# Optimization experiments

Measured on AMD Instinct MI355X. Metric: run time of the kernel, lower is better.

The kernel has to match this reference:

```python
import jax, jax.numpy as jnp
import numpy as np

B, S, D, H = 4, 2048, 1024, 16
HD = D // H  # head_size = 64


def setup_inputs() -> dict:
    key = jax.random.key(0)
    ks = jax.random.split(key, 9)
    sc = 0.02
    x = jax.random.normal(ks[0], (B, S, D), dtype=jnp.float32)
    Wq = jax.random.normal(ks[1], (H, D, HD), dtype=jnp.float32) * sc
    Wk = jax.random.normal(ks[2], (H, D, HD), dtype=jnp.float32) * sc
    Wv = jax.random.normal(ks[3], (H, D, HD), dtype=jnp.float32) * sc
    bq = jax.random.normal(ks[4], (H, HD), dtype=jnp.float32) * sc
    bk = jax.random.normal(ks[5], (H, HD), dtype=jnp.float32) * sc
    bv = jax.random.normal(ks[6], (H, HD), dtype=jnp.float32) * sc
    Wp = jax.random.normal(ks[7], (D, D), dtype=jnp.float32) * sc
    bp = jax.random.normal(ks[8], (D,), dtype=jnp.float32) * sc
    return {"x": x, "Wq": Wq, "bq": bq, "Wk": Wk, "bk": bk,
            "Wv": Wv, "bv": bv, "Wp": Wp, "bp": bp}


def reference(x, Wq, bq, Wk, bk, Wv, bv, Wp, bp):
    # Per-head Linear q/k/v, batched over heads with einsum (equivalent math
    # to the original Python loop over SingleHeadAttention modules).
    q = jnp.einsum('bsd,hde->bhse', x, Wq) + bq[None, :, None, :]
    k = jnp.einsum('bsd,hde->bhse', x, Wk) + bk[None, :, None, :]
    v = jnp.einsum('bsd,hde->bhse', x, Wv) + bv[None, :, None, :]
    att = jnp.einsum('bhqe,bhke->bhqk', q, k) / jnp.sqrt(jnp.asarray(HD, q.dtype))
    causal = jnp.tril(jnp.ones((S, S), dtype=bool))  # [S,S]
    att = jnp.where(causal[None, None], att, jnp.finfo(att.dtype).min)
    w = jax.nn.softmax(att, axis=-1)
    o = jnp.einsum('bhqk,bhke->bhqe', w, v)           # [B,H,S,HD]
    o = o.transpose(0, 2, 1, 3).reshape(B, S, D)      # concat heads on last dim
    # output projection; dropout is identity in eval (p=0.0)
    return jnp.einsum('bsd,de->bse', o, Wp) + bp
```

## Files before the change

### kernel.cpp

```cpp
#include <hip/hip_runtime.h>
#include <hip/hip_bf16.h>

typedef __attribute__((ext_vector_type(8)))  short bf16x8;
typedef __attribute__((ext_vector_type(4)))  float f32x4;
typedef __attribute__((ext_vector_type(16))) float f32x16;
typedef __attribute__((ext_vector_type(2)))  int   i32x2;

#define NH  16
#define HD  64
#define SEQ 2048
#define DM  1024
#define NB  4

#define QSCALE 0.18033688011112042f

#define MFMA(a,b,c)   __builtin_amdgcn_mfma_f32_16x16x32_bf16((a),(b),(c),0,0,0)
#define MFMA32(a,b,c) __builtin_amdgcn_mfma_f32_32x32x16_bf16((a),(b),(c),0,0,0)

static __device__ __forceinline__ void gload_lds16(const void* g, void* l) {
    __builtin_amdgcn_global_load_lds(
        (const __attribute__((address_space(1))) void*)g,
        (__attribute__((address_space(3))) void*)l, 16, 0, 0);
}

__global__ __launch_bounds__(256)
void prep(const float* __restrict__ x,  const float* __restrict__ Wq,
          const float* __restrict__ Wk, const float* __restrict__ Wv,
          const float* __restrict__ Wp,
          __hip_bfloat16* __restrict__ xb,  __hip_bfloat16* __restrict__ wqt,
          __hip_bfloat16* __restrict__ wkt, __hip_bfloat16* __restrict__ wvt,
          __hip_bfloat16* __restrict__ wpt) {
    const long XE = (long)NB * SEQ * DM;
    const long CAST_T = XE / 8;
    long gid = (long)blockIdx.x * 256 + threadIdx.x;
    if (gid < CAST_T) {
        long i = gid * 8;
        float4 a = *reinterpret_cast<const float4*>(x + i);
        float4 b = *reinterpret_cast<const float4*>(x + i + 4);
        ushort4 o1, o2;
        o1.x = __bfloat16_as_ushort(__float2bfloat16(a.x));
        o1.y = __bfloat16_as_ushort(__float2bfloat16(a.y));
        o1.z = __bfloat16_as_ushort(__float2bfloat16(a.z));
        o1.w = __bfloat16_as_ushort(__float2bfloat16(a.w));
        o2.x = __bfloat16_as_ushort(__float2bfloat16(b.x));
        o2.y = __bfloat16_as_ushort(__float2bfloat16(b.y));
        o2.z = __bfloat16_as_ushort(__float2bfloat16(b.z));
        o2.w = __bfloat16_as_ushort(__float2bfloat16(b.w));
        *reinterpret_cast<ushort4*>(xb + i)     = o1;
        *reinterpret_cast<ushort4*>(xb + i + 4) = o2;
        return;
    }
    long r = gid - CAST_T;
    const long WQK = 1 << 20;
    if (r < 3 * WQK) {
        int z = (int)(r >> 20);
        long idx = r & (WQK - 1);
        const float* src = (z == 0) ? Wq : (z == 1) ? Wk : Wv;
        __hip_bfloat16* dst = (z == 0) ? wqt : (z == 1) ? wkt : wvt;
        int c  = (int)(idx & 63);
        long t2 = idx >> 6;
        int rr = (int)(t2 & 1023);
        int mm = (int)(t2 >> 10);
        dst[((long)mm * HD + c) * DM + rr] = __float2bfloat16(src[idx]);
    } else {
        long idx = r - 3 * WQK;
        int c  = (int)(idx & 1023);
        int rr = (int)(idx >> 10);
        wpt[(long)c * DM + rr] = __float2bfloat16(Wp[idx]);
    }
}

__global__ __launch_bounds__(256)
void qkv_gemm(const __hip_bfloat16* __restrict__ A,
              const __hip_bfloat16* __restrict__ BT,
              const float* __restrict__ b0,
              const float* __restrict__ b1,
              const float* __restrict__ b2,
              __hip_bfloat16* __restrict__ Qo,
              __hip_bfloat16* __restrict__ Ko,
              __hip_bfloat16* __restrict__ Vto) {
    __shared__ __align__(16) char lds[2][32768];
    int tid = threadIdx.x;
    int w = tid >> 6, l = tid & 63;
    int lr = l & 15, lg = l >> 4;
    int wr = w >> 1, wc = w & 1;
    int mtile = blockIdx.x, ntile = blockIdx.y;
    const int AR0 = mtile * 128, BR0 = ntile * 128;

    const int rsub = w * 8 + (l >> 3);
    const int sg0 = l & 7;
    auto stage = [&](const __hip_bfloat16* g, int grow0, int kc, char* lbase) {
#pragma unroll
        for (int i = 0; i < 4; ++i) {
            int row = i * 32 + rsub;
            gload_lds16(g + (long)(grow0 + row) * DM + kc + ((sg0 ^ (row & 7)) << 3),
                        lbase + i * 4096 + w * 1024);
        }
    };

    int aoff[4][2], boff[4][2];
#pragma unroll
    for (int m = 0; m < 4; ++m) {
        int ra = wr * 64 + m * 16 + lr;
        int rb = wc * 64 + m * 16 + lr;
#pragma unroll
        for (int kh = 0; kh < 2; ++kh) {
            aoff[m][kh] = ra * 128 + (((kh * 4 + lg) ^ (ra & 7)) << 4);
            boff[m][kh] = 16384 + rb * 128 + (((kh * 4 + lg) ^ (rb & 7)) << 4);
        }
    }

    f32x4 acc[4][4] = {};

    stage(A,  AR0, 0, lds[0]);
    stage(BT, BR0, 0, lds[0] + 16384);
    __syncthreads();

    int cur = 0;
    for (int kt = 0; kt < 16; ++kt) {
        if (kt < 15) {
            int kc = (kt + 1) * 64;
            stage(A,  AR0, kc, lds[cur ^ 1]);
            stage(BT, BR0, kc, lds[cur ^ 1] + 16384);
        }
        bf16x8 bf[4][2];
#pragma unroll
        for (int n = 0; n < 4; ++n) {
            bf[n][0] = *(const bf16x8*)(lds[cur] + boff[n][0]);
            bf[n][1] = *(const bf16x8*)(lds[cur] + boff[n][1]);
        }
#pragma unroll
        for (int m = 0; m < 4; ++m) {
            bf16x8 a0 = *(const bf16x8*)(lds[cur] + aoff[m][0]);
            bf16x8 a1 = *(const bf16x8*)(lds[cur] + aoff[m][1]);
#pragma unroll
            for (int n = 0; n < 4; ++n) {
                acc[m][n] = MFMA(a0, bf[n][0], acc[m][n]);
                acc[m][n] = MFMA(a1, bf[n][1], acc[m][n]);
            }
        }
        __syncthreads();
        cur ^= 1;
    }

    int z = ntile >> 3;
    const float* bias = (z == 0) ? b0 : (z == 1) ? b1 : b2;
    int colbase = (ntile & 7) * 128 + wc * 64;
#pragma unroll
    for (int n = 0; n < 4; ++n) {
        int hc = colbase + n * 16 + lr;
        int h = hc >> 6, e = hc & 63;
        float bb = bias[hc];
#pragma unroll
        for (int m = 0; m < 4; ++m) {
            int row0 = mtile * 128 + wr * 64 + m * 16 + lg * 4;
            int b = row0 >> 11, s0 = row0 & 2047;
            if (z == 0) {
#pragma unroll
                for (int r = 0; r < 4; ++r)
                    Qo[(((long)b * NH + h) * SEQ + s0 + r) * HD + e] =
                        __float2bfloat16((acc[m][n][r] + bb) * QSCALE);
            } else if (z == 1) {
#pragma unroll
                for (int r = 0; r < 4; ++r)
                    Ko[(((long)b * NH + h) * SEQ + s0 + r) * HD + e] =
                        __float2bfloat16(acc[m][n][r] + bb);
            } else {
                ushort4 s4;
                s4.x = __bfloat16_as_ushort(__float2bfloat16(acc[m][n][0] + bb));
                s4.y = __bfloat16_as_ushort(__float2bfloat16(acc[m][n][1] + bb));
                s4.z = __bfloat16_as_ushort(__float2bfloat16(acc[m][n][2] + bb));
                s4.w = __bfloat16_as_ushort(__float2bfloat16(acc[m][n][3] + bb));
                *reinterpret_cast<ushort4*>(
                    Vto + ((long)(b * NH + h) * HD + e) * SEQ + s0) = s4;
            }
        }
    }
}

__global__ __launch_bounds__(256)
void out_gemm(const __hip_bfloat16* __restrict__ A,
              const __hip_bfloat16* __restrict__ BT,
              const float* __restrict__ b0,
              float* __restrict__ Fo) {
    __shared__ __align__(16) char smem[2][16384];
    int tid = threadIdx.x;
    int w = tid >> 6, l = tid & 63;
    int wr = w >> 1, wc = w & 1;
    int lr = l & 15, lg = l >> 4;
    int mtile = blockIdx.x, ntile = blockIdx.y;

    const __hip_bfloat16* Ab = A  + (long)mtile * 128 * DM;
    const __hip_bfloat16* Bb = BT + (long)ntile * 128 * DM;

    const int srow0 = tid >> 2;
    const int srow1 = 64 + srow0;
    const int g0 = (tid & 3) ^ ((srow0 >> 1) & 3);

    int aoff[4], boff[4];
#pragma unroll
    for (int m = 0; m < 4; ++m) {
        int ra = wr * 64 + m * 16 + lr;
        aoff[m] = ra * 64 + ((lg ^ ((ra >> 1) & 3)) * 16);
        int rb = wc * 64 + m * 16 + lr;
        boff[m] = 8192 + rb * 64 + ((lg ^ ((rb >> 1) & 3)) * 16);
    }

    f32x4 acc[4][4] = {};

    {
        char* base = smem[0] + w * 1024;
        gload_lds16(Ab + (long)srow0 * DM + g0 * 8, base);
        gload_lds16(Ab + (long)srow1 * DM + g0 * 8, base + 4096);
        gload_lds16(Bb + (long)srow0 * DM + g0 * 8, base + 8192);
        gload_lds16(Bb + (long)srow1 * DM + g0 * 8, base + 12288);
    }
    __syncthreads();

    int cur = 0;
    for (int kt = 0; kt < 32; ++kt) {
        if (kt != 31) {
            int k0 = (kt + 1) * 32;
            char* base = smem[cur ^ 1] + w * 1024;
            gload_lds16(Ab + (long)srow0 * DM + k0 + g0 * 8, base);
            gload_lds16(Ab + (long)srow1 * DM + k0 + g0 * 8, base + 4096);
            gload_lds16(Bb + (long)srow0 * DM + k0 + g0 * 8, base + 8192);
            gload_lds16(Bb + (long)srow1 * DM + k0 + g0 * 8, base + 12288);
        }
        bf16x8 af[4], bf[4];
#pragma unroll
        for (int m = 0; m < 4; ++m)
            af[m] = *reinterpret_cast<const bf16x8*>(smem[cur] + aoff[m]);
#pragma unroll
        for (int n = 0; n < 4; ++n)
            bf[n] = *reinterpret_cast<const bf16x8*>(smem[cur] + boff[n]);
#pragma unroll
        for (int m = 0; m < 4; ++m)
#pragma unroll
            for (int n = 0; n < 4; ++n)
                acc[m][n] = MFMA(af[m], bf[n], acc[m][n]);
        __syncthreads();
        cur ^= 1;
    }

#pragma unroll
    for (int n = 0; n < 4; ++n) {
        int col = ntile * 128 + wc * 64 + n * 16 + lr;
        float bb = b0[col];
#pragma unroll
        for (int m = 0; m < 4; ++m) {
            long row0 = mtile * 128 + wr * 64 + m * 16 + lg * 4;
#pragma unroll
            for (int r = 0; r < 4; ++r)
                Fo[(row0 + r) * DM + col] = acc[m][n][r] + bb;
        }
    }
}

static __device__ __forceinline__ unsigned pkbf(float a, float b) {
    __hip_bfloat162 h = __float22bfloat162_rn(float2{a, b});
    union { __hip_bfloat162 h2; unsigned u; } u_; u_.h2 = h;
    return u_.u;
}
static __device__ __forceinline__ bf16x8 make_pb(unsigned w0, unsigned w1,
                                                 unsigned w2, unsigned w3) {
    union { unsigned u[4]; bf16x8 v; } u_;
    u_.u[0] = w0; u_.u[1] = w1; u_.u[2] = w2; u_.u[3] = w3;
    return u_.v;
}
static __device__ __forceinline__ i32x2 pl32swap(unsigned a, unsigned b) {
    return __builtin_amdgcn_permlane32_swap((int)a, (int)b, false, false);
}
static __device__ __forceinline__ float xsum32(float x) {
    i32x2 r = pl32swap(__float_as_uint(x), __float_as_uint(x));
    return __uint_as_float((unsigned)r[0]) + __uint_as_float((unsigned)r[1]);
}

template<bool MASKED>
static __device__ __forceinline__ void attn_tile(
    const bf16x8* kf, const bf16x8* qf, const bf16x8* vf,
    int lo5, int hi,
    f32x16& o0, f32x16& o1, float& lsum) {
    f32x16 st = {};
    __builtin_amdgcn_s_setprio(1);
#pragma unroll
    for (int kd = 0; kd < 4; ++kd) st = MFMA32(kf[kd], qf[kd], st);
    __builtin_amdgcn_s_setprio(0);
    if (MASKED) {
#pragma unroll
        for (int r = 0; r < 16; ++r) {
            int kvloc = (r & 3) + 8 * (r >> 2) + 4 * hi;
            st[r] = (kvloc > lo5) ? -INFINITY : st[r];
        }
    }
    float p[16];
#pragma unroll
    for (int r = 0; r < 16; ++r) p[r] = __builtin_amdgcn_exp2f(st[r]);
    float s0 = (p[0] + p[1]) + (p[2] + p[3]);
    float s1 = (p[4] + p[5]) + (p[6] + p[7]);
    float s2 = (p[8] + p[9]) + (p[10] + p[11]);
    float s3 = (p[12] + p[13]) + (p[14] + p[15]);
    lsum += xsum32((s0 + s1) + (s2 + s3));

    unsigned pk0 = pkbf(p[0],  p[1]),  pk1 = pkbf(p[2],  p[3]);
    unsigned pk2 = pkbf(p[4],  p[5]),  pk3 = pkbf(p[6],  p[7]);
    unsigned pk4 = pkbf(p[8],  p[9]),  pk5 = pkbf(p[10], p[11]);
    unsigned pk6 = pkbf(p[12], p[13]), pk7 = pkbf(p[14], p[15]);
    i32x2 s02 = pl32swap(pk0, pk2);
    i32x2 s13 = pl32swap(pk1, pk3);
    i32x2 s46 = pl32swap(pk4, pk6);
    i32x2 s57 = pl32swap(pk5, pk7);
    bf16x8 pb0 = make_pb((unsigned)s02[0], (unsigned)s13[0],
                         (unsigned)s02[1], (unsigned)s13[1]);
    bf16x8 pb1 = make_pb((unsigned)s46[0], (unsigned)s57[0],
                         (unsigned)s46[1], (unsigned)s57[1]);

    __builtin_amdgcn_s_setprio(1);
    o0 = MFMA32(vf[0], pb0, o0);
    o1 = MFMA32(vf[1], pb0, o1);
    o0 = MFMA32(vf[2], pb1, o0);
    o1 = MFMA32(vf[3], pb1, o1);
    __builtin_amdgcn_s_setprio(0);
}

__global__ __launch_bounds__(256)
void flash_attn(const __hip_bfloat16* __restrict__ Q,
                const __hip_bfloat16* __restrict__ K,
                const __hip_bfloat16* __restrict__ Vt,
                __hip_bfloat16* __restrict__ O) {
    int bh = blockIdx.x;
    int w  = threadIdx.x >> 6, l = threadIdx.x & 63;
    int lo5 = l & 31, hi = l >> 5;
    int pair = blockIdx.y * 4 + w;
    int jA = pair, jB = 63 - pair;
    int q0A = jA * 32, q0B = jB * 32;

    const __hip_bfloat16* Qh = Q  + (long)bh * SEQ * HD;
    const __hip_bfloat16* Kh = K  + (long)bh * SEQ * HD;
    const __hip_bfloat16* Vh = Vt + (long)bh * HD * SEQ;

    bf16x8 qfA[4], qfB[4];
#pragma unroll
    for (int kd = 0; kd < 4; ++kd) {
        qfA[kd] = *reinterpret_cast<const bf16x8*>(
            Qh + (long)(q0A + lo5) * HD + kd * 16 + hi * 8);
        qfB[kd] = *reinterpret_cast<const bf16x8*>(
            Qh + (long)(q0B + lo5) * HD + kd * 16 + hi * 8);
    }

    f32x16 oA0 = {}, oA1 = {}, oB0 = {}, oB1 = {};
    float lsA = 0.f, lsB = 0.f;

    bf16x8 k0[4], k1[4], v0[4], v1[4];

#define LOADK(T, DST)                                                      \
    _Pragma("unroll")                                                      \
    for (int kd = 0; kd < 4; ++kd)                                         \
        DST[kd] = *reinterpret_cast<const bf16x8*>(                        \
            Kh + (long)((T) * 32 + lo5) * HD + kd * 16 + hi * 8);

#define LOADV(T, DST)                                                      \
    DST[0] = *reinterpret_cast<const bf16x8*>(                             \
        Vh + (long)(lo5) * SEQ + (T) * 32 + hi * 8);                       \
    DST[1] = *reinterpret_cast<const bf16x8*>(                             \
        Vh + (long)(32 + lo5) * SEQ + (T) * 32 + hi * 8);                  \
    DST[2] = *reinterpret_cast<const bf16x8*>(                             \
        Vh + (long)(lo5) * SEQ + (T) * 32 + 16 + hi * 8);                  \
    DST[3] = *reinterpret_cast<const bf16x8*>(                             \
        Vh + (long)(32 + lo5) * SEQ + (T) * 32 + 16 + hi * 8);

#define TILE_B(KK, VV)  attn_tile<false>(KK, qfB, VV, lo5, hi, oB0, oB1, lsB)
#define TILE_A(KK, VV)  attn_tile<false>(KK, qfA, VV, lo5, hi, oA0, oA1, lsA)
#define DIAG_A(KK, VV)  attn_tile<true >(KK, qfA, VV, lo5, hi, oA0, oA1, lsA)
#define DIAG_B(KK, VV)  attn_tile<true >(KK, qfB, VV, lo5, hi, oB0, oB1, lsB)

#define PHASE2(KA_, VA_, KB_, VB_)                                         \
    {                                                                      \
        int u = jA + 1;                                                    \
        while (u + 1 < jB) {                                               \
            LOADK(u + 1, KB_); LOADV(u + 1, VB_);                          \
            TILE_B(KA_, VA_);                                              \
            LOADK(u + 2, KA_); LOADV(u + 2, VA_);                          \
            TILE_B(KB_, VB_);                                              \
            u += 2;                                                        \
        }                                                                  \
        if (u < jB) {                                                      \
            LOADK(jB, KB_); LOADV(jB, VB_);                                \
            TILE_B(KA_, VA_);                                              \
            DIAG_B(KB_, VB_);                                              \
        } else {                                                           \
            DIAG_B(KA_, VA_);                                              \
        }                                                                  \
    }

    LOADK(0, k0); LOADV(0, v0);

    int t = 0;
    while (t + 1 < jA) {
        LOADK(t + 1, k1); LOADV(t + 1, v1);
        TILE_B(k0, v0);
        TILE_A(k0, v0);
        LOADK(t + 2, k0); LOADV(t + 2, v0);
        TILE_B(k1, v1);
        TILE_A(k1, v1);
        t += 2;
    }
    if (t < jA) {
        LOADK(jA, k1); LOADV(jA, v1);
        TILE_B(k0, v0);
        TILE_A(k0, v0);
        LOADK(jA + 1, k0); LOADV(jA + 1, v0);
        DIAG_A(k1, v1);
        TILE_B(k1, v1);
        PHASE2(k0, v0, k1, v1)
    } else {
        LOADK(jA + 1, k1); LOADV(jA + 1, v1);
        DIAG_A(k0, v0);
        TILE_B(k0, v0);
        PHASE2(k1, v1, k0, v0)
    }

#undef LOADK
#undef LOADV
#undef TILE_B
#undef TILE_A
#undef DIAG_A
#undef DIAG_B
#undef PHASE2

    int b = bh >> 4, h = bh & 15;
#pragma unroll
    for (int c = 0; c < 2; ++c) {
        int q0 = c ? q0B : q0A;
        const f32x16& o0 = c ? oB0 : oA0;
        const f32x16& o1 = c ? oB1 : oA1;
        float inv = 1.0f / (c ? lsB : lsA);
        __hip_bfloat16* orow = O + ((long)b * SEQ + q0 + lo5) * DM + h * HD;
#pragma unroll
        for (int nd = 0; nd < 2; ++nd) {
#pragma unroll
            for (int rg = 0; rg < 4; ++rg) {
                ushort4 s4;
                float a0 = (nd ? o1[rg * 4 + 0] : o0[rg * 4 + 0]) * inv;
                float a1 = (nd ? o1[rg * 4 + 1] : o0[rg * 4 + 1]) * inv;
                float a2 = (nd ? o1[rg * 4 + 2] : o0[rg * 4 + 2]) * inv;
                float a3 = (nd ? o1[rg * 4 + 3] : o0[rg * 4 + 3]) * inv;
                s4.x = __bfloat16_as_ushort(__float2bfloat16(a0));
                s4.y = __bfloat16_as_ushort(__float2bfloat16(a1));
                s4.z = __bfloat16_as_ushort(__float2bfloat16(a2));
                s4.w = __bfloat16_as_ushort(__float2bfloat16(a3));
                *reinterpret_cast<ushort4*>(orow + nd * 32 + rg * 8 + hi * 4) = s4;
            }
        }
    }
}

extern "C" void kernel_launch(void* const* d_in, const int* in_sizes, int n_in,
                              void* d_out, int out_size, void* d_ws, size_t ws_size,
                              hipStream_t stream) {
    const float* x  = (const float*)d_in[0];
    const float* Wq = (const float*)d_in[1];
    const float* bq = (const float*)d_in[2];
    const float* Wk = (const float*)d_in[3];
    const float* bk = (const float*)d_in[4];
    const float* Wv = (const float*)d_in[5];
    const float* bv = (const float*)d_in[6];
    const float* Wp = (const float*)d_in[7];
    const float* bp = (const float*)d_in[8];
    float* out = (float*)d_out;

    char* ws = (char*)d_ws;
    const long XE = (long)NB * SEQ * DM;
    const long QKV_ELEMS = (long)NB * NH * SEQ * HD;
    __hip_bfloat16* xb   = (__hip_bfloat16*)ws; ws += XE * 2;
    __hip_bfloat16* Qws  = (__hip_bfloat16*)ws; ws += QKV_ELEMS * 2;
    __hip_bfloat16* Kws  = (__hip_bfloat16*)ws; ws += QKV_ELEMS * 2;
    __hip_bfloat16* Vtws = (__hip_bfloat16*)ws; ws += QKV_ELEMS * 2;
    __hip_bfloat16* Ows  = (__hip_bfloat16*)ws; ws += QKV_ELEMS * 2;
    __hip_bfloat16* wqt  = (__hip_bfloat16*)ws; ws += (long)NH * DM * HD * 2;
    __hip_bfloat16* wkt  = (__hip_bfloat16*)ws; ws += (long)NH * DM * HD * 2;
    __hip_bfloat16* wvt  = (__hip_bfloat16*)ws; ws += (long)NH * DM * HD * 2;
    __hip_bfloat16* wpt  = (__hip_bfloat16*)ws; ws += (long)DM * DM * 2;

    prep<<<20480, 256, 0, stream>>>(x, Wq, Wk, Wv, Wp, xb, wqt, wkt, wvt, wpt);

    qkv_gemm<<<dim3(64, 24), 256, 0, stream>>>(
        xb, wqt, bq, bk, bv, Qws, Kws, Vtws);

    flash_attn<<<dim3(64, 8), 256, 0, stream>>>(Qws, Kws, Vtws, Ows);

    out_gemm<<<dim3(64, 8), 256, 0, stream>>>(Ows, wpt, bp, out);
}
```

Measured before the change: 219.8 us.

## Share K/V tiles across waves via double-buffered LDS and defer row-sum reduction

Each wave previously loaded its own K and V tiles straight from global memory into registers. Now the four waves of a block cooperatively stage each 32-row K/V tile into swizzled, double-buffered shared memory with direct global-to-LDS loads, prefetching the next tile while computing the current one. Each wave reads its fragments from LDS and skips tiles outside its causal range. The cross-lane row-sum reduction moves out of the inner loop and runs once at the end. In exchange, every tile now needs a block-wide barrier, so waves with little work wait for the wave with the longest range.

```diff
diff --git a/kernel.cpp b/kernel.cpp
--- a/kernel.cpp
+++ b/kernel.cpp
@@ -300,7 +300,7 @@
     float s1 = (p[4] + p[5]) + (p[6] + p[7]);
     float s2 = (p[8] + p[9]) + (p[10] + p[11]);
     float s3 = (p[12] + p[13]) + (p[14] + p[15]);
-    lsum += xsum32((s0 + s1) + (s2 + s3));
+    lsum += (s0 + s1) + (s2 + s3);
 
     unsigned pk0 = pkbf(p[0],  p[1]),  pk1 = pkbf(p[2],  p[3]);
     unsigned pk2 = pkbf(p[4],  p[5]),  pk3 = pkbf(p[6],  p[7]);
@@ -328,12 +328,15 @@
                 const __hip_bfloat16* __restrict__ K,
                 const __hip_bfloat16* __restrict__ Vt,
                 __hip_bfloat16* __restrict__ O) {
+    __shared__ __align__(16) char kv[2][8192];
     int bh = blockIdx.x;
     int w  = threadIdx.x >> 6, l = threadIdx.x & 63;
     int lo5 = l & 31, hi = l >> 5;
-    int pair = blockIdx.y * 4 + w;
-    int jA = pair, jB = 63 - pair;
+    int y  = blockIdx.y;
+    int pr = y * 4 + w;
+    int jA = pr, jB = 63 - pr;
     int q0A = jA * 32, q0B = jB * 32;
+    const int TMAX = 63 - 4 * y;
 
     const __hip_bfloat16* Qh = Q  + (long)bh * SEQ * HD;
     const __hip_bfloat16* Kh = K  + (long)bh * SEQ * HD;
@@ -348,93 +351,68 @@
             Qh + (long)(q0B + lo5) * HD + kd * 16 + hi * 8);
     }
 
+    int srow = w * 8 + (l >> 3);
+    int kslot = (l & 7) ^ (srow & 7);
+    const __hip_bfloat16* ksrc = Kh + (long)srow * HD + kslot * 8;
+    int vlog = (l & 7) ^ (srow & 7);
+    int vrow = srow + ((vlog >> 2) << 5);
+    const __hip_bfloat16* vsrc = Vh + (long)vrow * SEQ + (vlog & 3) * 8;
+
+    int ka[4], va[4];
+#pragma unroll
+    for (int kd = 0; kd < 4; ++kd)
+        ka[kd] = lo5 * 128 + (((kd * 2 + hi) ^ (lo5 & 7)) << 4);
+    va[0] = 4096 + lo5 * 128 + (((0 + hi) ^ (lo5 & 7)) << 4);
+    va[1] = 4096 + lo5 * 128 + (((4 + hi) ^ (lo5 & 7)) << 4);
+    va[2] = 4096 + lo5 * 128 + (((2 + hi) ^ (lo5 & 7)) << 4);
+    va[3] = 4096 + lo5 * 128 + (((6 + hi) ^ (lo5 & 7)) << 4);
+
     f32x16 oA0 = {}, oA1 = {}, oB0 = {}, oB1 = {};
     float lsA = 0.f, lsB = 0.f;
 
-    bf16x8 k0[4], k1[4], v0[4], v1[4];
-
-#define LOADK(T, DST)                                                      \
-    _Pragma("unroll")                                                      \
-    for (int kd = 0; kd < 4; ++kd)                                         \
-        DST[kd] = *reinterpret_cast<const bf16x8*>(                        \
-            Kh + (long)((T) * 32 + lo5) * HD + kd * 16 + hi * 8);
-
-#define LOADV(T, DST)                                                      \
-    DST[0] = *reinterpret_cast<const bf16x8*>(                             \
-        Vh + (long)(lo5) * SEQ + (T) * 32 + hi * 8);                       \
-    DST[1] = *reinterpret_cast<const bf16x8*>(                             \
-        Vh + (long)(32 + lo5) * SEQ + (T) * 32 + hi * 8);                  \
-    DST[2] = *reinterpret_cast<const bf16x8*>(                             \
-        Vh + (long)(lo5) * SEQ + (T) * 32 + 16 + hi * 8);                  \
-    DST[3] = *reinterpret_cast<const bf16x8*>(                             \
-        Vh + (long)(32 + lo5) * SEQ + (T) * 32 + 16 + hi * 8);
-
-#define TILE_B(KK, VV)  attn_tile<false>(KK, qfB, VV, lo5, hi, oB0, oB1, lsB)
-#define TILE_A(KK, VV)  attn_tile<false>(KK, qfA, VV, lo5, hi, oA0, oA1, lsA)
-#define DIAG_A(KK, VV)  attn_tile<true >(KK, qfA, VV, lo5, hi, oA0, oA1, lsA)
-#define DIAG_B(KK, VV)  attn_tile<true >(KK, qfB, VV, lo5, hi, oB0, oB1, lsB)
-
-#define PHASE2(KA_, VA_, KB_, VB_)                                         \
-    {                                                                      \
-        int u = jA + 1;                                                    \
-        while (u + 1 < jB) {                                               \
-            LOADK(u + 1, KB_); LOADV(u + 1, VB_);                          \
-            TILE_B(KA_, VA_);                                              \
-            LOADK(u + 2, KA_); LOADV(u + 2, VA_);                          \
-            TILE_B(KB_, VB_);                                              \
-            u += 2;                                                        \
-        }                                                                  \
-        if (u < jB) {                                                      \
-            LOADK(jB, KB_); LOADV(jB, VB_);                                \
-            TILE_B(KA_, VA_);                                              \
-            DIAG_B(KB_, VB_);                                              \
-        } else {                                                           \
-            DIAG_B(KA_, VA_);                                              \
-        }                                                                  \
-    }
-
-    LOADK(0, k0); LOADV(0, v0);
-
-    int t = 0;
-    while (t + 1 < jA) {
-        LOADK(t + 1, k1); LOADV(t + 1, v1);
-        TILE_B(k0, v0);
-        TILE_A(k0, v0);
-        LOADK(t + 2, k0); LOADV(t + 2, v0);
-        TILE_B(k1, v1);
-        TILE_A(k1, v1);
-        t += 2;
-    }
-    if (t < jA) {
-        LOADK(jA, k1); LOADV(jA, v1);
-        TILE_B(k0, v0);
-        TILE_A(k0, v0);
-        LOADK(jA + 1, k0); LOADV(jA + 1, v0);
-        DIAG_A(k1, v1);
-        TILE_B(k1, v1);
-        PHASE2(k0, v0, k1, v1)
-    } else {
-        LOADK(jA + 1, k1); LOADV(jA + 1, v1);
-        DIAG_A(k0, v0);
-        TILE_B(k0, v0);
-        PHASE2(k1, v1, k0, v0)
-    }
-
-#undef LOADK
-#undef LOADV
-#undef TILE_B
-#undef TILE_A
-#undef DIAG_A
-#undef DIAG_B
-#undef PHASE2
+    gload_lds16(ksrc, kv[0] + w * 1024);
+    gload_lds16(vsrc, kv[0] + 4096 + w * 1024);
+    __syncthreads();
+
+    int buf = 0;
+    for (int t = 0; t <= TMAX; ++t) {
+        if (t < TMAX) {
+            gload_lds16(ksrc + (long)(t + 1) * 32 * HD, kv[buf ^ 1] + w * 1024);
+            gload_lds16(vsrc + (t + 1) * 32,            kv[buf ^ 1] + 4096 + w * 1024);
+        }
+        const char* cb = kv[buf];
+        bf16x8 kf[4], vf[4];
+#pragma unroll
+        for (int kd = 0; kd < 4; ++kd)
+            kf[kd] = *reinterpret_cast<const bf16x8*>(cb + ka[kd]);
+#pragma unroll
+        for (int j = 0; j < 4; ++j)
+            vf[j] = *reinterpret_cast<const bf16x8*>(cb + va[j]);
+
+        if (t < jA) {
+            attn_tile<false>(kf, qfB, vf, lo5, hi, oB0, oB1, lsB);
+            attn_tile<false>(kf, qfA, vf, lo5, hi, oA0, oA1, lsA);
+        } else if (t == jA) {
+            attn_tile<true >(kf, qfA, vf, lo5, hi, oA0, oA1, lsA);
+            attn_tile<false>(kf, qfB, vf, lo5, hi, oB0, oB1, lsB);
+        } else if (t < jB) {
+            attn_tile<false>(kf, qfB, vf, lo5, hi, oB0, oB1, lsB);
+        } else if (t == jB) {
+            attn_tile<true >(kf, qfB, vf, lo5, hi, oB0, oB1, lsB);
+        }
+        __syncthreads();
+        buf ^= 1;
+    }
 
     int b = bh >> 4, h = bh & 15;
+    float invA = 1.0f / xsum32(lsA);
+    float invB = 1.0f / xsum32(lsB);
 #pragma unroll
     for (int c = 0; c < 2; ++c) {
         int q0 = c ? q0B : q0A;
         const f32x16& o0 = c ? oB0 : oA0;
         const f32x16& o1 = c ? oB1 : oA1;
-        float inv = 1.0f / (c ? lsB : lsA);
+        float inv = c ? invB : invA;
         __hip_bfloat16* orow = O + ((long)b * SEQ + q0 + lo5) * DM + h * HD;
 #pragma unroll
         for (int nd = 0; nd < 2; ++nd) {
```

New measurement: 185.4 us. -15.7%, faster.
